# Kernel optimization log

Hardware: AMD Instinct MI355X
Metric: run time of the kernel (lower is better)

Reference implementation:

```python
import jax, jax.numpy as jnp
import numpy as np

N_HEAD, D_K, D_V, EPS = 8, 64, 64, 1e-6


def setup_inputs() -> dict:
    key = jax.random.key(0)
    ks = jax.random.split(key, 7)
    b, n, t, d = 8, 4, 512, 512
    q = jax.random.normal(ks[0], (b, n, t, d), dtype=jnp.float32)
    k = jax.random.normal(ks[1], (b, n, t, d), dtype=jnp.float32)
    v = jax.random.normal(ks[2], (b, n, t, d), dtype=jnp.float32)
    s = 1.0 / np.sqrt(d)
    w_q = jax.random.normal(ks[3], (N_HEAD * D_K, d), dtype=jnp.float32) * s
    w_k = jax.random.normal(ks[4], (N_HEAD * D_K, d), dtype=jnp.float32) * s
    w_v = jax.random.normal(ks[5], (N_HEAD * D_V, d), dtype=jnp.float32) * s
    w_fc = jax.random.normal(ks[6], (d, N_HEAD * D_V), dtype=jnp.float32) * s
    ln_gamma = jnp.ones((d,), dtype=jnp.float32)
    ln_beta = jnp.zeros((d,), dtype=jnp.float32)
    return {"q": q, "k": k, "v": v, "w_q": w_q, "w_k": w_k, "w_v": w_v,
            "w_fc": w_fc, "ln_gamma": ln_gamma, "ln_beta": ln_beta}


def reference(q, k, v, w_q, w_k, w_v, w_fc, ln_gamma, ln_beta):
    b, n, t, d = q.shape
    B = b * n
    qf = q.reshape(B, t, d)
    kf = k.reshape(B, t, d)
    vf = v.reshape(B, t, d)
    residual = qf
    # projections -> [B, H, T, dk/dv]
    Q = jnp.einsum('btd,ed->bte', qf, w_q).reshape(B, t, N_HEAD, D_K).transpose(0, 2, 1, 3)
    K = jnp.einsum('btd,ed->bte', kf, w_k).reshape(B, t, N_HEAD, D_K).transpose(0, 2, 1, 3)
    V = jnp.einsum('btd,ed->bte', vf, w_v).reshape(B, t, N_HEAD, D_V).transpose(0, 2, 1, 3)
    # scaled dot-product attention (scale by sqrt(d_k) of q's last dim)
    scale = 1.0 / jnp.sqrt(jnp.asarray(D_K, dtype=Q.dtype))
    attn = jax.nn.softmax(jnp.einsum('bhqd,bhkd->bhqk', Q * scale, K), axis=-1)
    O = jnp.einsum('bhqk,bhkd->bhqd', attn, V)  # [B, H, T, dv]
    # merge heads, then the original's extra transpose+view (layout scramble)
    x = O.transpose(0, 2, 1, 3).reshape(B, t, N_HEAD * D_V)
    x = jnp.transpose(x, (0, 2, 1)).reshape(B, t, N_HEAD * D_V)
    x = jnp.einsum('bte,de->btd', x, w_fc)
    x = x + residual
    # LayerNorm(eps=1e-6)
    mu = jnp.mean(x, axis=-1, keepdims=True)
    var = jnp.var(x, axis=-1, keepdims=True)
    x = (x - mu) * jax.lax.rsqrt(var + EPS) * ln_gamma + ln_beta
    return x.reshape(b, n, t, d)
```

## Files before the change

kernel.cpp:

```cpp
#include <hip/hip_runtime.h>
#include <hip/hip_bf16.h>
#include <stdint.h>

typedef __attribute__((ext_vector_type(8))) short bf16x8;
typedef __attribute__((ext_vector_type(4))) float f32x4;
typedef unsigned int u32;

#define MFMA16(a,b,c) __builtin_amdgcn_mfma_f32_16x16x32_bf16((a),(b),(c),0,0,0)

__device__ __forceinline__ unsigned short f2bf(float f) {
    unsigned u = __float_as_uint(f);
    u = (u + 0x7FFFu + ((u >> 16) & 1u)) >> 16;
    return (unsigned short)u;
}
__device__ __forceinline__ float bf2f(unsigned short h) {
    return __uint_as_float(((unsigned)h) << 16);
}
__device__ __forceinline__ void gload16(const unsigned short* gp, unsigned short* lp) {
    __builtin_amdgcn_global_load_lds(
        (const __attribute__((address_space(1))) u32*)gp,
        (__attribute__((address_space(3))) u32*)lp, 16, 0, 0);
}


__global__ __launch_bounds__(256) void prep_kernel(
    const float* __restrict__ q, const float* __restrict__ k, const float* __restrict__ v,
    const float* __restrict__ wq, const float* __restrict__ wk, const float* __restrict__ wv,
    const float* __restrict__ wfc,
    unsigned short* __restrict__ Xq, unsigned short* __restrict__ Xk, unsigned short* __restrict__ Xv,
    unsigned short* __restrict__ Wcat)
{
    const long total = 3276800;
    for (long c = (long)blockIdx.x * 256 + threadIdx.x; c < total; c += (long)gridDim.x * 256) {
        const float* src;
        unsigned short* dst;
        long off;
        if (c < 3145728) {
            int t = (int)(c >> 20);
            off = (c & 1048575) * 8;
            src = (t == 0) ? q : (t == 1) ? k : v;
            dst = (t == 0) ? Xq : (t == 1) ? Xk : Xv;
        } else {
            long c2 = c - 3145728;
            int w = (int)(c2 >> 15);
            off = (c2 & 32767) * 8;
            src = (w == 0) ? wq : (w == 1) ? wk : (w == 2) ? wv : wfc;
            dst = Wcat + (long)w * 262144;
        }
        const float4 a = *(const float4*)(src + off);
        const float4 b = *(const float4*)(src + off + 4);
        uint4 pk;
        pk.x = (u32)f2bf(a.x) | ((u32)f2bf(a.y) << 16);
        pk.y = (u32)f2bf(a.z) | ((u32)f2bf(a.w) << 16);
        pk.z = (u32)f2bf(b.x) | ((u32)f2bf(b.y) << 16);
        pk.w = (u32)f2bf(b.z) | ((u32)f2bf(b.w) << 16);
        *(uint4*)(dst + off) = pk;
    }
}

__device__ __forceinline__ void gemm_body(
    const unsigned short* __restrict__ A, const unsigned short* __restrict__ Bm,
    unsigned short* __restrict__ out, int mode, float scale,
    unsigned short* As, unsigned short* Bs, int m0, int n0)
{
    const int tid = threadIdx.x, wid = tid >> 6, lane = tid & 63;
    const int wm = wid >> 1, wn = wid & 1;
    const int g = lane >> 4, cc = lane & 15;

    f32x4 acc[4][4];
    #pragma unroll
    for (int a = 0; a < 4; a++)
        #pragma unroll
        for (int b = 0; b < 4; b++)
            acc[a][b] = (f32x4){0.f, 0.f, 0.f, 0.f};

    for (int k0 = 0; k0 < 512; k0 += 64) {
        #pragma unroll
        for (int j = 0; j < 4; j++) {
            const int sb = j * 256 + wid * 64;
            const int s = sb + lane;
            const int r = s >> 3, cs = s & 7;
            const int cd = cs ^ (r & 7);
            gload16(A  + (size_t)(m0 + r) * 512 + k0 + cd * 8, As + (size_t)sb * 8);
            gload16(Bm + (size_t)(n0 + r) * 512 + k0 + cd * 8, Bs + (size_t)sb * 8);
        }
        __syncthreads();

        #pragma unroll
        for (int kc = 0; kc < 2; kc++) {
            bf16x8 af[4], bfr[4];
            #pragma unroll
            for (int mf = 0; mf < 4; mf++) {
                const int r = wm * 64 + mf * 16 + cc;
                af[mf] = *(const bf16x8*)(As + r * 64 + (((kc * 4 + g) ^ (r & 7)) * 8));
            }
            #pragma unroll
            for (int nf = 0; nf < 4; nf++) {
                const int r = wn * 64 + nf * 16 + cc;
                bfr[nf] = *(const bf16x8*)(Bs + r * 64 + (((kc * 4 + g) ^ (r & 7)) * 8));
            }
            __builtin_amdgcn_s_setprio(1);
            #pragma unroll
            for (int mf = 0; mf < 4; mf++)
                #pragma unroll
                for (int nf = 0; nf < 4; nf++)
                    acc[mf][nf] = MFMA16(af[mf], bfr[nf], acc[mf][nf]);
            __builtin_amdgcn_s_setprio(0);
        }
        __syncthreads();
    }

    #pragma unroll
    for (int mf = 0; mf < 4; mf++) {
        const int rg = m0 + wm * 64 + mf * 16 + g * 4;
        const int t0 = rg & 511, bI = rg >> 9;
        #pragma unroll
        for (int nf = 0; nf < 4; nf++) {
            const int col = n0 + wn * 64 + nf * 16 + cc;
            if (mode == 0) {
                const int h = col >> 6, dd = col & 63;
                const size_t base = ((size_t)((bI * 8 + h) * 512 + t0)) * 64 + dd;
                #pragma unroll
                for (int i = 0; i < 4; i++)
                    out[base + (size_t)i * 64] = f2bf(acc[mf][nf][i] * scale);
            } else if (mode == 1) {
                const int h = col >> 6, dd = col & 63;
                const size_t base = ((size_t)((bI * 8 + h) * 64 + dd)) * 512 + t0;
                uint2 pk;
                pk.x = (u32)f2bf(acc[mf][nf][0]) | ((u32)f2bf(acc[mf][nf][1]) << 16);
                pk.y = (u32)f2bf(acc[mf][nf][2]) | ((u32)f2bf(acc[mf][nf][3]) << 16);
                *(uint2*)(out + base) = pk;
            } else {
                #pragma unroll
                for (int i = 0; i < 4; i++)
                    out[(size_t)(rg + i) * 512 + col] = f2bf(acc[mf][nf][i]);
            }
        }
    }
}

__global__ __launch_bounds__(256) void proj_kernel(
    const unsigned short* __restrict__ Xq, const unsigned short* __restrict__ Xk,
    const unsigned short* __restrict__ Xv, const unsigned short* __restrict__ Wcat,
    unsigned short* __restrict__ Qb, unsigned short* __restrict__ Kb,
    unsigned short* __restrict__ Vt)
{
    __shared__ __align__(16) unsigned short As[128 * 64];
    __shared__ __align__(16) unsigned short Bs[128 * 64];
    const int z = blockIdx.z;
    const unsigned short* A = (z == 0) ? Xq : (z == 1) ? Xk : Xv;
    const unsigned short* B = Wcat + (size_t)z * 262144;
    unsigned short* out = (z == 0) ? Qb : (z == 1) ? Kb : Vt;
    const int mode = (z == 2) ? 1 : 0;
    const float scale = (z == 0) ? 0.125f : 1.0f;
    gemm_body(A, B, out, mode, scale, As, Bs, blockIdx.y * 128, blockIdx.x * 128);
}

__global__ __launch_bounds__(256) void fc_kernel(
    const unsigned short* __restrict__ Os, const unsigned short* __restrict__ Wfc,
    unsigned short* __restrict__ Y)
{
    __shared__ __align__(16) unsigned short As[128 * 64];
    __shared__ __align__(16) unsigned short Bs[128 * 64];
    gemm_body(Os, Wfc, Y, 2, 1.0f, As, Bs, blockIdx.y * 128, blockIdx.x * 128);
}

__global__ __launch_bounds__(256) void attn_kernel(
    const unsigned short* __restrict__ Qb, const unsigned short* __restrict__ Kb,
    const unsigned short* __restrict__ Vt, unsigned short* __restrict__ Os)
{
    __shared__ __align__(16) unsigned short Ks[64 * 64];
    __shared__ __align__(16) unsigned short Vs[64 * 64];
    __shared__ __align__(16) unsigned short Ps[4 * 32 * 64];

    const int bh = blockIdx.x;
    const int qt = blockIdx.y;
    const int tid = threadIdx.x;
    const int wid = tid >> 6, lane = tid & 63;
    const int g = lane >> 4, cc = lane & 15;

    const unsigned short* Qp = Qb + (size_t)bh * 512 * 64;
    const unsigned short* Kp = Kb + (size_t)bh * 512 * 64;
    const unsigned short* Vp = Vt + (size_t)bh * 64 * 512;

    const int q0 = qt * 128 + wid * 32;

    bf16x8 qf[2][2];
    #pragma unroll
    for (int mf = 0; mf < 2; mf++)
        #pragma unroll
        for (int kb = 0; kb < 2; kb++)
            qf[mf][kb] = *(const bf16x8*)(Qp + (size_t)(q0 + mf * 16 + cc) * 64 + kb * 32 + g * 8);

    f32x4 o[2][4];
    #pragma unroll
    for (int a = 0; a < 2; a++)
        #pragma unroll
        for (int b = 0; b < 4; b++)
            o[a][b] = (f32x4){0.f, 0.f, 0.f, 0.f};
    float lrun[2][4];
    #pragma unroll
    for (int a = 0; a < 2; a++)
        #pragma unroll
        for (int i = 0; i < 4; i++) lrun[a][i] = 0.f;

    const int sb = wid * 64;
    const int s1 = sb + lane, r1 = s1 >> 3, cd1 = (s1 & 7) ^ (r1 & 7);
    const int s2 = sb + 256 + lane, r2 = s2 >> 3, cd2 = (s2 & 7) ^ (r2 & 7);

    for (int kt = 0; kt < 8; kt++) {
        gload16(Kp + (size_t)(kt * 64 + r1) * 64 + cd1 * 8, Ks + (size_t)sb * 8);
        gload16(Kp + (size_t)(kt * 64 + r2) * 64 + cd2 * 8, Ks + (size_t)(sb + 256) * 8);
        gload16(Vp + (size_t)r1 * 512 + kt * 64 + cd1 * 8, Vs + (size_t)sb * 8);
        gload16(Vp + (size_t)r2 * 512 + kt * 64 + cd2 * 8, Vs + (size_t)(sb + 256) * 8);
        __syncthreads();

        f32x4 s[2][4];
        #pragma unroll
        for (int a = 0; a < 2; a++)
            #pragma unroll
            for (int b = 0; b < 4; b++)
                s[a][b] = (f32x4){0.f, 0.f, 0.f, 0.f};
        __builtin_amdgcn_s_setprio(1);
        #pragma unroll
        for (int nf = 0; nf < 4; nf++) {
            const int r = nf * 16 + cc;
            #pragma unroll
            for (int kb = 0; kb < 2; kb++) {
                bf16x8 kf = *(const bf16x8*)(Ks + r * 64 + (((kb * 4 + g) ^ (r & 7)) * 8));
                s[0][nf] = MFMA16(qf[0][kb], kf, s[0][nf]);
                s[1][nf] = MFMA16(qf[1][kb], kf, s[1][nf]);
            }
        }
        __builtin_amdgcn_s_setprio(0);

        unsigned short* Pw = Ps + wid * 32 * 64;
        #pragma unroll
        for (int mf = 0; mf < 2; mf++)
            #pragma unroll
            for (int i = 0; i < 4; i++) {
                float lacc = 0.f;
                #pragma unroll
                for (int nf = 0; nf < 4; nf++) {
                    float p = __expf(s[mf][nf][i]);
                    s[mf][nf][i] = p;
                    lacc += p;
                }
                lrun[mf][i] += lacc;
            }

        #pragma unroll
        for (int mf = 0; mf < 2; mf++)
            #pragma unroll
            for (int nf = 0; nf < 4; nf++) {
                const int c = nf * 16 + cc, csl = c >> 3, cin = c & 7;
                #pragma unroll
                for (int i = 0; i < 4; i++) {
                    const int row = mf * 16 + g * 4 + i;
                    Pw[row * 64 + ((csl ^ (row & 7)) * 8) + cin] = f2bf(s[mf][nf][i]);
                }
            }

        __builtin_amdgcn_s_setprio(1);
        #pragma unroll
        for (int kc = 0; kc < 2; kc++) {
            bf16x8 pa[2], vb[4];
            #pragma unroll
            for (int mf = 0; mf < 2; mf++) {
                const int r = mf * 16 + cc;
                pa[mf] = *(const bf16x8*)(Pw + r * 64 + (((kc * 4 + g) ^ (r & 7)) * 8));
            }
            #pragma unroll
            for (int vf = 0; vf < 4; vf++) {
                const int r = vf * 16 + cc;
                vb[vf] = *(const bf16x8*)(Vs + r * 64 + (((kc * 4 + g) ^ (r & 7)) * 8));
            }
            #pragma unroll
            for (int mf = 0; mf < 2; mf++)
                #pragma unroll
                for (int vf = 0; vf < 4; vf++)
                    o[mf][vf] = MFMA16(pa[mf], vb[vf], o[mf][vf]);
        }
        __builtin_amdgcn_s_setprio(0);
        __syncthreads();
    }

    const int b = bh >> 3, h = bh & 7;
    #pragma unroll
    for (int mf = 0; mf < 2; mf++) {
        int tq0 = q0 + mf * 16 + g * 4;
        float inv[4];
        #pragma unroll
        for (int i = 0; i < 4; i++) {
            float l = lrun[mf][i];
            #pragma unroll
            for (int d = 1; d < 16; d <<= 1) l += __shfl_xor(l, d);
            inv[i] = 1.0f / l;
        }
        #pragma unroll
        for (int vf = 0; vf < 4; vf++) {
            int dv = vf * 16 + cc;
            uint2 pk;
            pk.x = (u32)f2bf(o[mf][vf][0] * inv[0]) | ((u32)f2bf(o[mf][vf][1] * inv[1]) << 16);
            pk.y = (u32)f2bf(o[mf][vf][2] * inv[2]) | ((u32)f2bf(o[mf][vf][3] * inv[3]) << 16);
            size_t base = ((size_t)b * 512 + h * 64 + dv) * 512 + tq0;
            *(uint2*)(Os + base) = pk;
        }
    }
}

__global__ __launch_bounds__(256) void ln_kernel(
    const unsigned short* __restrict__ y, const float* __restrict__ resid,
    const float* __restrict__ gamma, const float* __restrict__ beta,
    float* __restrict__ out)
{
    const int wid = threadIdx.x >> 6, lane = threadIdx.x & 63;
    const int row = blockIdx.x * 4 + wid;
    const unsigned short* yr = y + (size_t)row * 512;
    const float* rr = resid + (size_t)row * 512;

    const bf16x8 yv = *(const bf16x8*)(yr + lane * 8);
    const float4 r0 = *(const float4*)(rr + lane * 8);
    const float4 r1 = *(const float4*)(rr + lane * 8 + 4);
    float x[8];
    x[0] = bf2f((unsigned short)yv[0]) + r0.x;
    x[1] = bf2f((unsigned short)yv[1]) + r0.y;
    x[2] = bf2f((unsigned short)yv[2]) + r0.z;
    x[3] = bf2f((unsigned short)yv[3]) + r0.w;
    x[4] = bf2f((unsigned short)yv[4]) + r1.x;
    x[5] = bf2f((unsigned short)yv[5]) + r1.y;
    x[6] = bf2f((unsigned short)yv[6]) + r1.z;
    x[7] = bf2f((unsigned short)yv[7]) + r1.w;

    float s = 0.f, sq = 0.f;
    #pragma unroll
    for (int j = 0; j < 8; j++) { s += x[j]; sq += x[j] * x[j]; }
    #pragma unroll
    for (int d = 1; d < 64; d <<= 1) {
        s += __shfl_xor(s, d);
        sq += __shfl_xor(sq, d);
    }
    const float mu = s * (1.0f / 512.0f);
    const float var = sq * (1.0f / 512.0f) - mu * mu;
    const float rs = rsqrtf(var + 1e-6f);

    #pragma unroll
    for (int j = 0; j < 2; j++) {
        const int colb = lane * 8 + j * 4;
        const float4 gg = *(const float4*)(gamma + colb);
        const float4 bb = *(const float4*)(beta + colb);
        float4 ov;
        ov.x = (x[j * 4 + 0] - mu) * rs * gg.x + bb.x;
        ov.y = (x[j * 4 + 1] - mu) * rs * gg.y + bb.y;
        ov.z = (x[j * 4 + 2] - mu) * rs * gg.z + bb.z;
        ov.w = (x[j * 4 + 3] - mu) * rs * gg.w + bb.w;
        *(float4*)(out + (size_t)row * 512 + colb) = ov;
    }
}

extern "C" void kernel_launch(void* const* d_in, const int* in_sizes, int n_in,
                              void* d_out, int out_size, void* d_ws, size_t ws_size,
                              hipStream_t stream) {
    const float* q     = (const float*)d_in[0];
    const float* k     = (const float*)d_in[1];
    const float* v     = (const float*)d_in[2];
    const float* wq    = (const float*)d_in[3];
    const float* wk    = (const float*)d_in[4];
    const float* wv    = (const float*)d_in[5];
    const float* wfc   = (const float*)d_in[6];
    const float* gamma = (const float*)d_in[7];
    const float* beta  = (const float*)d_in[8];
    float* out = (float*)d_out;

    char* ws = (char*)d_ws;
    const size_t SEG = 16777216;
    unsigned short* Xq   = (unsigned short*)(ws);
    unsigned short* Xk   = (unsigned short*)(ws + SEG);
    unsigned short* Xv   = (unsigned short*)(ws + 2 * SEG);
    unsigned short* Qb   = (unsigned short*)(ws + 3 * SEG);
    unsigned short* Vt   = (unsigned short*)(ws + 4 * SEG);
    unsigned short* Wcat = (unsigned short*)(ws + 5 * SEG);
    unsigned short* Kb = Xq;
    unsigned short* Os = Xk;
    unsigned short* Y  = Xv;

    prep_kernel<<<2048, 256, 0, stream>>>(q, k, v, wq, wk, wv, wfc, Xq, Xk, Xv, Wcat);
    proj_kernel<<<dim3(4, 128, 3), 256, 0, stream>>>(Xq, Xk, Xv, Wcat, Qb, Kb, Vt);
    attn_kernel<<<dim3(256, 4), 256, 0, stream>>>(Qb, Kb, Vt, Os);
    fc_kernel<<<dim3(4, 128), 256, 0, stream>>>(Os, Wcat + 786432, Y);
    ln_kernel<<<4096, 256, 0, stream>>>(Y, q, gamma, beta, out);
}
```

Baseline: 139.6 us.

## Double-buffer LDS tiles, swizzle blocks across XCDs, use bf16 residual in LayerNorm

The projection/FC GEMM and the attention kernel now keep two LDS buffers, so the next K/V or A/B tile is loaded while MFMAs run on the current one. Block indices are remapped so neighbouring tiles land on the same XCD, which is meant to improve L2 reuse. When the workspace is large enough, K gets its own buffer and LayerNorm reads the bf16 copy of q as the residual instead of the fp32 original, cutting its memory traffic. In exchange, LDS per block doubles, which may lower occupancy, and the bf16 residual adds rounding error.

```diff
diff --git a/kernel.cpp b/kernel.cpp
--- a/kernel.cpp
+++ b/kernel.cpp
@@ -20,6 +20,9 @@
     __builtin_amdgcn_global_load_lds(
         (const __attribute__((address_space(1))) u32*)gp,
         (__attribute__((address_space(3))) u32*)lp, 16, 0, 0);
+}
+__device__ __forceinline__ int xcd_swz(int bid, int q8) {
+    return (bid & 7) * q8 + (bid >> 3);
 }
 
 
@@ -61,7 +64,9 @@
 __device__ __forceinline__ void gemm_body(
     const unsigned short* __restrict__ A, const unsigned short* __restrict__ Bm,
     unsigned short* __restrict__ out, int mode, float scale,
-    unsigned short* As, unsigned short* Bs, int m0, int n0)
+    unsigned short* As0, unsigned short* Bs0,
+    unsigned short* As1, unsigned short* Bs1,
+    int m0, int n0)
 {
     const int tid = threadIdx.x, wid = tid >> 6, lane = tid & 63;
     const int wm = wid >> 1, wn = wid & 1;
@@ -74,17 +79,27 @@
         for (int b = 0; b < 4; b++)
             acc[a][b] = (f32x4){0.f, 0.f, 0.f, 0.f};
 
-    for (int k0 = 0; k0 < 512; k0 += 64) {
+    auto STAGE = [&](unsigned short* As, unsigned short* Bs, int k0) {
         #pragma unroll
         for (int j = 0; j < 4; j++) {
             const int sb = j * 256 + wid * 64;
             const int s = sb + lane;
-            const int r = s >> 3, cs = s & 7;
-            const int cd = cs ^ (r & 7);
+            const int r = s >> 3;
+            const int cd = (s & 7) ^ (r & 7);
             gload16(A  + (size_t)(m0 + r) * 512 + k0 + cd * 8, As + (size_t)sb * 8);
             gload16(Bm + (size_t)(n0 + r) * 512 + k0 + cd * 8, Bs + (size_t)sb * 8);
         }
-        __syncthreads();
+    };
+
+    STAGE(As0, Bs0, 0);
+    __syncthreads();
+
+    #pragma unroll
+    for (int t = 0; t < 8; t++) {
+        unsigned short* Ac = (t & 1) ? As1 : As0;
+        unsigned short* Bc = (t & 1) ? Bs1 : Bs0;
+        if (t < 7)
+            STAGE((t & 1) ? As0 : As1, (t & 1) ? Bs0 : Bs1, (t + 1) * 64);
 
         #pragma unroll
         for (int kc = 0; kc < 2; kc++) {
@@ -92,12 +107,12 @@
             #pragma unroll
             for (int mf = 0; mf < 4; mf++) {
                 const int r = wm * 64 + mf * 16 + cc;
-                af[mf] = *(const bf16x8*)(As + r * 64 + (((kc * 4 + g) ^ (r & 7)) * 8));
+                af[mf] = *(const bf16x8*)(Ac + r * 64 + (((kc * 4 + g) ^ (r & 7)) * 8));
             }
             #pragma unroll
             for (int nf = 0; nf < 4; nf++) {
                 const int r = wn * 64 + nf * 16 + cc;
-                bfr[nf] = *(const bf16x8*)(Bs + r * 64 + (((kc * 4 + g) ^ (r & 7)) * 8));
+                bfr[nf] = *(const bf16x8*)(Bc + r * 64 + (((kc * 4 + g) ^ (r & 7)) * 8));
             }
             __builtin_amdgcn_s_setprio(1);
             #pragma unroll
@@ -145,36 +160,39 @@
     unsigned short* __restrict__ Qb, unsigned short* __restrict__ Kb,
     unsigned short* __restrict__ Vt)
 {
-    __shared__ __align__(16) unsigned short As[128 * 64];
-    __shared__ __align__(16) unsigned short Bs[128 * 64];
-    const int z = blockIdx.z;
+    __shared__ __align__(16) unsigned short As[2][128 * 64];
+    __shared__ __align__(16) unsigned short Bs[2][128 * 64];
+    const int work = xcd_swz(blockIdx.x, 192);
+    const int x = work & 3, y = (work >> 2) & 127, z = work >> 9;
     const unsigned short* A = (z == 0) ? Xq : (z == 1) ? Xk : Xv;
     const unsigned short* B = Wcat + (size_t)z * 262144;
     unsigned short* out = (z == 0) ? Qb : (z == 1) ? Kb : Vt;
     const int mode = (z == 2) ? 1 : 0;
     const float scale = (z == 0) ? 0.125f : 1.0f;
-    gemm_body(A, B, out, mode, scale, As, Bs, blockIdx.y * 128, blockIdx.x * 128);
+    gemm_body(A, B, out, mode, scale, As[0], Bs[0], As[1], Bs[1], y * 128, x * 128);
 }
 
 __global__ __launch_bounds__(256) void fc_kernel(
     const unsigned short* __restrict__ Os, const unsigned short* __restrict__ Wfc,
     unsigned short* __restrict__ Y)
 {
-    __shared__ __align__(16) unsigned short As[128 * 64];
-    __shared__ __align__(16) unsigned short Bs[128 * 64];
-    gemm_body(Os, Wfc, Y, 2, 1.0f, As, Bs, blockIdx.y * 128, blockIdx.x * 128);
+    __shared__ __align__(16) unsigned short As[2][128 * 64];
+    __shared__ __align__(16) unsigned short Bs[2][128 * 64];
+    const int work = xcd_swz(blockIdx.x, 64);
+    const int x = work & 3, y = work >> 2;
+    gemm_body(Os, Wfc, Y, 2, 1.0f, As[0], Bs[0], As[1], Bs[1], y * 128, x * 128);
 }
 
 __global__ __launch_bounds__(256) void attn_kernel(
     const unsigned short* __restrict__ Qb, const unsigned short* __restrict__ Kb,
     const unsigned short* __restrict__ Vt, unsigned short* __restrict__ Os)
 {
-    __shared__ __align__(16) unsigned short Ks[64 * 64];
-    __shared__ __align__(16) unsigned short Vs[64 * 64];
+    __shared__ __align__(16) unsigned short Ks[2][64 * 64];
+    __shared__ __align__(16) unsigned short Vs[2][64 * 64];
     __shared__ __align__(16) unsigned short Ps[4 * 32 * 64];
 
-    const int bh = blockIdx.x;
-    const int qt = blockIdx.y;
+    const int work = xcd_swz(blockIdx.x, 128);
+    const int qt = work & 3, bh = work >> 2;
     const int tid = threadIdx.x;
     const int wid = tid >> 6, lane = tid & 63;
     const int g = lane >> 4, cc = lane & 15;
@@ -208,12 +226,20 @@
     const int s1 = sb + lane, r1 = s1 >> 3, cd1 = (s1 & 7) ^ (r1 & 7);
     const int s2 = sb + 256 + lane, r2 = s2 >> 3, cd2 = (s2 & 7) ^ (r2 & 7);
 
+    auto STAGEKV = [&](int buf, int kt) {
+        gload16(Kp + (size_t)(kt * 64 + r1) * 64 + cd1 * 8, Ks[buf] + (size_t)sb * 8);
+        gload16(Kp + (size_t)(kt * 64 + r2) * 64 + cd2 * 8, Ks[buf] + (size_t)(sb + 256) * 8);
+        gload16(Vp + (size_t)r1 * 512 + kt * 64 + cd1 * 8, Vs[buf] + (size_t)sb * 8);
+        gload16(Vp + (size_t)r2 * 512 + kt * 64 + cd2 * 8, Vs[buf] + (size_t)(sb + 256) * 8);
+    };
+
+    STAGEKV(0, 0);
+    __syncthreads();
+
+    #pragma unroll
     for (int kt = 0; kt < 8; kt++) {
-        gload16(Kp + (size_t)(kt * 64 + r1) * 64 + cd1 * 8, Ks + (size_t)sb * 8);
-        gload16(Kp + (size_t)(kt * 64 + r2) * 64 + cd2 * 8, Ks + (size_t)(sb + 256) * 8);
-        gload16(Vp + (size_t)r1 * 512 + kt * 64 + cd1 * 8, Vs + (size_t)sb * 8);
-        gload16(Vp + (size_t)r2 * 512 + kt * 64 + cd2 * 8, Vs + (size_t)(sb + 256) * 8);
-        __syncthreads();
+        const int cur = kt & 1;
+        if (kt < 7) STAGEKV(cur ^ 1, kt + 1);
 
         f32x4 s[2][4];
         #pragma unroll
@@ -227,7 +253,7 @@
             const int r = nf * 16 + cc;
             #pragma unroll
             for (int kb = 0; kb < 2; kb++) {
-                bf16x8 kf = *(const bf16x8*)(Ks + r * 64 + (((kb * 4 + g) ^ (r & 7)) * 8));
+                bf16x8 kf = *(const bf16x8*)(Ks[cur] + r * 64 + (((kb * 4 + g) ^ (r & 7)) * 8));
                 s[0][nf] = MFMA16(qf[0][kb], kf, s[0][nf]);
                 s[1][nf] = MFMA16(qf[1][kb], kf, s[1][nf]);
             }
@@ -273,7 +299,7 @@
             #pragma unroll
             for (int vf = 0; vf < 4; vf++) {
                 const int r = vf * 16 + cc;
-                vb[vf] = *(const bf16x8*)(Vs + r * 64 + (((kc * 4 + g) ^ (r & 7)) * 8));
+                vb[vf] = *(const bf16x8*)(Vs[cur] + r * 64 + (((kc * 4 + g) ^ (r & 7)) * 8));
             }
             #pragma unroll
             for (int mf = 0; mf < 2; mf++)
@@ -310,27 +336,35 @@
 }
 
 __global__ __launch_bounds__(256) void ln_kernel(
-    const unsigned short* __restrict__ y, const float* __restrict__ resid,
+    const unsigned short* __restrict__ y, const unsigned short* __restrict__ residb,
+    const float* __restrict__ residf,
     const float* __restrict__ gamma, const float* __restrict__ beta,
-    float* __restrict__ out)
+    float* __restrict__ out, int use_bf16_resid)
 {
     const int wid = threadIdx.x >> 6, lane = threadIdx.x & 63;
     const int row = blockIdx.x * 4 + wid;
     const unsigned short* yr = y + (size_t)row * 512;
-    const float* rr = resid + (size_t)row * 512;
 
     const bf16x8 yv = *(const bf16x8*)(yr + lane * 8);
-    const float4 r0 = *(const float4*)(rr + lane * 8);
-    const float4 r1 = *(const float4*)(rr + lane * 8 + 4);
     float x[8];
-    x[0] = bf2f((unsigned short)yv[0]) + r0.x;
-    x[1] = bf2f((unsigned short)yv[1]) + r0.y;
-    x[2] = bf2f((unsigned short)yv[2]) + r0.z;
-    x[3] = bf2f((unsigned short)yv[3]) + r0.w;
-    x[4] = bf2f((unsigned short)yv[4]) + r1.x;
-    x[5] = bf2f((unsigned short)yv[5]) + r1.y;
-    x[6] = bf2f((unsigned short)yv[6]) + r1.z;
-    x[7] = bf2f((unsigned short)yv[7]) + r1.w;
+    if (use_bf16_resid) {
+        const bf16x8 rv = *(const bf16x8*)(residb + (size_t)row * 512 + lane * 8);
+        #pragma unroll
+        for (int j = 0; j < 8; j++)
+            x[j] = bf2f((unsigned short)yv[j]) + bf2f((unsigned short)rv[j]);
+    } else {
+        const float* rr = residf + (size_t)row * 512;
+        const float4 r0 = *(const float4*)(rr + lane * 8);
+        const float4 r1 = *(const float4*)(rr + lane * 8 + 4);
+        x[0] = bf2f((unsigned short)yv[0]) + r0.x;
+        x[1] = bf2f((unsigned short)yv[1]) + r0.y;
+        x[2] = bf2f((unsigned short)yv[2]) + r0.z;
+        x[3] = bf2f((unsigned short)yv[3]) + r0.w;
+        x[4] = bf2f((unsigned short)yv[4]) + r1.x;
+        x[5] = bf2f((unsigned short)yv[5]) + r1.y;
+        x[6] = bf2f((unsigned short)yv[6]) + r1.z;
+        x[7] = bf2f((unsigned short)yv[7]) + r1.w;
+    }
 
     float s = 0.f, sq = 0.f;
     #pragma unroll
@@ -374,19 +408,32 @@
 
     char* ws = (char*)d_ws;
     const size_t SEG = 16777216;
-    unsigned short* Xq   = (unsigned short*)(ws);
-    unsigned short* Xk   = (unsigned short*)(ws + SEG);
-    unsigned short* Xv   = (unsigned short*)(ws + 2 * SEG);
-    unsigned short* Qb   = (unsigned short*)(ws + 3 * SEG);
-    unsigned short* Vt   = (unsigned short*)(ws + 4 * SEG);
-    unsigned short* Wcat = (unsigned short*)(ws + 5 * SEG);
-    unsigned short* Kb = Xq;
-    unsigned short* Os = Xk;
-    unsigned short* Y  = Xv;
+    const bool big = ws_size >= 6 * SEG + 2097152;
+
+    unsigned short *Xq, *Xk, *Xv, *Qb, *Kb, *Vt, *Os, *Y, *Wcat;
+    if (big) {
+        Xq = (unsigned short*)(ws);
+        Xk = (unsigned short*)(ws + SEG);
+        Xv = (unsigned short*)(ws + 2 * SEG);
+        Qb = (unsigned short*)(ws + 3 * SEG);
+        Kb = (unsigned short*)(ws + 4 * SEG);
+        Vt = (unsigned short*)(ws + 5 * SEG);
+        Wcat = (unsigned short*)(ws + 6 * SEG);
+        Os = Xk; Y = Xv;
+    } else {
+        Xq = (unsigned short*)(ws);
+        Xk = (unsigned short*)(ws + SEG);
+        Xv = (unsigned short*)(ws + 2 * SEG);
+        Qb = (unsigned short*)(ws + 3 * SEG);
+        Vt = (unsigned short*)(ws + 4 * SEG);
+        Wcat = (unsigned short*)(ws + 5 * SEG);
+        Kb = Xq; Os = Xk; Y = Xv;
+    }
 
     prep_kernel<<<2048, 256, 0, stream>>>(q, k, v, wq, wk, wv, wfc, Xq, Xk, Xv, Wcat);
-    proj_kernel<<<dim3(4, 128, 3), 256, 0, stream>>>(Xq, Xk, Xv, Wcat, Qb, Kb, Vt);
-    attn_kernel<<<dim3(256, 4), 256, 0, stream>>>(Qb, Kb, Vt, Os);
-    fc_kernel<<<dim3(4, 128), 256, 0, stream>>>(Os, Wcat + 786432, Y);
-    ln_kernel<<<4096, 256, 0, stream>>>(Y, q, gamma, beta, out);
-}
+    proj_kernel<<<1536, 256, 0, stream>>>(Xq, Xk, Xv, Wcat, Qb, Kb, Vt);
+    attn_kernel<<<1024, 256, 0, stream>>>(Qb, Kb, Vt, Os);
+    fc_kernel<<<512, 256, 0, stream>>>(Os, Wcat + 786432, Y);
+    ln_kernel<<<4096, 256, 0, stream>>>(Y, big ? Xq : (unsigned short*)nullptr, q,
+                                        gamma, beta, out, big ? 1 : 0);
+}
```

After: 147.6 us. 1.06x slower.
